# Kernel optimization log

Measured on AMD Instinct MI355X. Metric: run time of the kernel, lower is better.

Reference implementation:

```python
import jax, jax.numpy as jnp
import numpy as np

K_GAUSS = 10
HIDDEN = 512


def setup_inputs() -> dict:
    key = jax.random.key(0)
    k1, k2, k3 = jax.random.split(key, 3)
    lstm_out = jax.random.normal(k1, (16, 1024, HIDDEN), dtype=jnp.float32)
    char_seq = jax.random.uniform(k2, (16, 600, 80), dtype=jnp.float32)
    # Dense(3*k_gaussians): small init so exp(params) stays in a sane range
    W = jax.random.normal(k3, (HIDDEN, 3 * K_GAUSS), dtype=jnp.float32) * 0.02
    bias = jnp.zeros((3 * K_GAUSS,), dtype=jnp.float32)
    return {"lstm_out": lstm_out, "char_seq": char_seq, "W": W, "bias": bias}


def reference(lstm_out, char_seq, W, bias):
    # lstm_out: [B,T,H], char_seq: [B,U,A]
    U = char_seq.shape[1]
    params = jnp.einsum('bth,hp->btp', lstm_out, W) + bias  # [B,T,3K]
    exp_params = jnp.exp(params)
    a, b, k = jnp.split(exp_params, 3, axis=2)              # each [B,T,K]
    u = jnp.arange(U, dtype=lstm_out.dtype).reshape(1, 1, U, 1)  # char indices
    # gaussian mixture window weights phi[b,t,u] = sum_k a*exp(-b*(k-u)^2)
    gaussians = a[:, :, None, :] * jnp.exp(-b[:, :, None, :] * jnp.square(k[:, :, None, :] - u))  # [B,T,U,K]
    char_weights = jnp.sum(gaussians, axis=3)               # [B,T,U]
    # alphabet_window[b,t,a] = sum_u phi[b,t,u] * char_seq[b,u,a]
    return jnp.einsum('btu,bua->bta', char_weights, char_seq)
```

## Files before the change

kernel.cpp:

```cpp
#include <hip/hip_runtime.h>
#include <math.h>

#define BB 16
#define TD 1024
#define HD 512
#define UD 600
#define AD 80
#define KG 10
#define PC 30
#define PP 32

#define LOG2E 1.4426950408889634f

#if __has_builtin(__builtin_amdgcn_exp2f)
#define EXP2F(x) __builtin_amdgcn_exp2f(x)
#else
#define EXP2F(x) exp2f(x)
#endif

typedef short v8s __attribute__((ext_vector_type(8)));
typedef float v4f __attribute__((ext_vector_type(4)));

__device__ inline unsigned short f2bf(float f) {
    unsigned u = __float_as_uint(f);
    return (unsigned short)((u + 0x7FFF + ((u >> 16) & 1)) >> 16);
}

__global__ void k_wprep(const float* __restrict__ W,
                        unsigned short* __restrict__ Wfh,
                        unsigned short* __restrict__ Wfl) {
    int p = blockIdx.x * 256 + threadIdx.x;
    for (; p < 32768; p += 256 * 32) {
        int j = p & 7, l = (p >> 3) & 63, n = (p >> 9) & 1, kt = p >> 10;
        int k = kt * 32 + ((l >> 4) * 8) + j;
        int c = n * 16 + (l & 15);
        float v = (c < PC) ? W[k * PC + c] : 0.f;
        unsigned short h = f2bf(v);
        float hi_f = __uint_as_float(((unsigned)h) << 16);
        Wfh[p] = h;
        Wfl[p] = f2bf(v - hi_f);
    }
}

#define TT 16
#define UC 40
#define NCHUNK 15
#define NTHR 320

__global__ __launch_bounds__(NTHR, 4) void k_fused(const float* __restrict__ x,
                                                   const unsigned short* __restrict__ Wfh,
                                                   const unsigned short* __restrict__ Wfl,
                                                   const float* __restrict__ bias,
                                                   const float* __restrict__ cs,
                                                   float* __restrict__ out) {
    __shared__ float red[4 * TT * 33];
    __shared__ float params_l[TT * 36];
    __shared__ float cs_l[UC * AD];
    __shared__ float phi2[TT * 44];
    __shared__ float range_l[2];

    int tid = threadIdx.x;
    int b = blockIdx.y;
    int t0 = blockIdx.x * TT;
    long r0 = (long)b * TD + t0;

    int wv = tid >> 6;
    int l = tid & 63;
    int quad = l >> 4, m = l & 15;

    const float* csb = cs + (long)b * UD * AD;

    if (wv < 4) {
        v4f acc[2] = {{0.f, 0.f, 0.f, 0.f}, {0.f, 0.f, 0.f, 0.f}};

        #pragma unroll
        for (int kt = 0; kt < 4; kt++) {
            int g = wv * 4 + kt;
            const float* xr = x + (r0 + m) * HD + g * 32 + quad * 8;
            float4 xa = *(const float4*)(xr);
            float4 xb = *(const float4*)(xr + 4);
            float xf[8] = {xa.x, xa.y, xa.z, xa.w, xb.x, xb.y, xb.z, xb.w};
            v8s ah, al;
            #pragma unroll
            for (int j = 0; j < 8; j++) {
                unsigned short h = f2bf(xf[j]);
                ah[j] = (short)h;
                al[j] = (short)f2bf(xf[j] - __uint_as_float(((unsigned)h) << 16));
            }
            #pragma unroll
            for (int n = 0; n < 2; n++) {
                uint4 uh = *(const uint4*)&Wfh[((g * 2 + n) * 64 + l) * 8];
                uint4 ul = *(const uint4*)&Wfl[((g * 2 + n) * 64 + l) * 8];
                v8s bh, bl;
                __builtin_memcpy(&bh, &uh, 16);
                __builtin_memcpy(&bl, &ul, 16);
                acc[n] = __builtin_amdgcn_mfma_f32_16x16x32_bf16(ah, bh, acc[n], 0, 0, 0);
                acc[n] = __builtin_amdgcn_mfma_f32_16x16x32_bf16(al, bh, acc[n], 0, 0, 0);
                acc[n] = __builtin_amdgcn_mfma_f32_16x16x32_bf16(ah, bl, acc[n], 0, 0, 0);
            }
        }

        #pragma unroll
        for (int n = 0; n < 2; n++)
            #pragma unroll
            for (int r = 0; r < 4; r++)
                red[wv * (TT * 33) + (quad * 4 + r) * 33 + n * 16 + m] = acc[n][r];
    } else {
        for (int idx = l; idx < (UC * AD) / 4; idx += 64)
            *(float4*)&cs_l[idx * 4] = *(const float4*)&csb[idx * 4];
    }
    __syncthreads();

    for (int idx = tid; idx < TT * PC; idx += NTHR) {
        int r = idx / PC, c = idx - r * PC;
        float s = red[0 * (TT * 33) + r * 33 + c] + red[1 * (TT * 33) + r * 33 + c]
                + red[2 * (TT * 33) + r * 33 + c] + red[3 * (TT * 33) + r * 33 + c];
        float e = __expf(s + bias[c]);
        params_l[r * 36 + c] = (c >= 10 && c < 20) ? (-e * LOG2E) : e;
    }
    __syncthreads();

    int tt = tid & 15;
    int sub = tid >> 4;
    float pa[KG], pnb[KG], pk[KG];
    #pragma unroll
    for (int q = 0; q < KG; q++) {
        pa[q]  = params_l[tt * 36 + q];
        pnb[q] = params_l[tt * 36 + 10 + q];
        pk[q]  = params_l[tt * 36 + 20 + q];
    }

    {
        float lo = 1e30f, hi = -1e30f;
        #pragma unroll
        for (int q = 0; q < KG; q++) {
            float bits = 46.f + fmaxf(0.f, __log2f(pa[q]));
            float w = __fsqrt_rn(bits / (-pnb[q]));
            lo = fminf(lo, pk[q] - w);
            hi = fmaxf(hi, pk[q] + w);
        }
        if (tid < 64) {
            #pragma unroll
            for (int mk = 1; mk < 64; mk <<= 1) {
                lo = fminf(lo, __shfl_xor(lo, mk));
                hi = fmaxf(hi, __shfl_xor(hi, mk));
            }
            if (tid == 0) { range_l[0] = lo; range_l[1] = hi; }
        }
    }
    __syncthreads();
    float lo_m = fminf(fmaxf(range_l[0], 0.f), (float)(UD - 1));
    float hi_m = fminf(fmaxf(range_l[1], 0.f), (float)(UD - 1));
    int ch_lo = (int)lo_m / UC;
    int ch_hi = (int)hi_m / UC;
    if (ch_lo > ch_hi) ch_lo = ch_hi;

    int tx = tid % 20;
    int ty = tid / 20;
    float4 acc0 = {0.f, 0.f, 0.f, 0.f};

    for (int ch = ch_lo; ch <= ch_hi; ch++) {
        int u0 = ch * UC;
        __syncthreads();

        if (ch != 0) {
            for (int idx = tid; idx < (UC * AD) / 4; idx += NTHR) {
                *(float4*)&cs_l[idx * 4] = *(const float4*)&csb[u0 * AD + idx * 4];
            }
        }

        float ph[2];
        #pragma unroll
        for (int i = 0; i < 2; i++) {
            float uf = (float)(u0 + sub * 2 + i);
            float ss = 0.f;
            #pragma unroll
            for (int q = 0; q < KG; q++) {
                float d = uf - pk[q];
                ss += pa[q] * EXP2F(pnb[q] * d * d);
            }
            ph[i] = ss;
        }
        *(float2*)&phi2[tt * 44 + sub * 2] = make_float2(ph[0], ph[1]);
        __syncthreads();

        #pragma unroll 2
        for (int g = 0; g < 10; g++) {
            float4 p0 = *(const float4*)&phi2[ty * 44 + g * 4];
            #pragma unroll
            for (int i = 0; i < 4; i++) {
                float4 c4 = *(const float4*)&cs_l[(g * 4 + i) * AD + tx * 4];
                float pi0 = (i == 0) ? p0.x : (i == 1) ? p0.y : (i == 2) ? p0.z : p0.w;
                acc0.x += pi0 * c4.x; acc0.y += pi0 * c4.y;
                acc0.z += pi0 * c4.z; acc0.w += pi0 * c4.w;
            }
        }
    }

    *(float4*)(out + (r0 + ty) * AD + tx * 4) = acc0;
}

extern "C" void kernel_launch(void* const* d_in, const int* in_sizes, int n_in,
                              void* d_out, int out_size, void* d_ws, size_t ws_size,
                              hipStream_t stream) {
    const float* lstm = (const float*)d_in[0];
    const float* cs   = (const float*)d_in[1];
    const float* W    = (const float*)d_in[2];
    const float* bias = (const float*)d_in[3];
    float* out = (float*)d_out;

    unsigned short* Wfh = (unsigned short*)d_ws;
    unsigned short* Wfl = Wfh + 32768;

    k_wprep<<<32, 256, 0, stream>>>(W, Wfh, Wfl);
    dim3 grid(TD / TT, BB);
    k_fused<<<grid, NTHR, 0, stream>>>(lstm, Wfh, Wfl, bias, cs, out);
}
```

Before: 89.60 us.

## Fold W bf16 split into fused kernel and drop separate prep launch

Removes the k_wprep kernel that pre-split W into bf16 hi/lo fragments, and instead has each MFMA wave load fp32 W directly and split it in-register. The MFMA operand roles are swapped (W as A, x as B), so the accumulator is transposed and the reduction buffer layout changes to match. The bf16 conversion now uses packed hardware conversion. This saves a kernel launch and the workspace round trip, at the cost of strided scalar W loads and redundant conversion work in every block.

Result: no change. 90.54 us (+1.0%).

```diff
diff --git a/kernel.cpp b/kernel.cpp
--- a/kernel.cpp
+++ b/kernel.cpp
@@ -1,4 +1,5 @@
 #include <hip/hip_runtime.h>
+#include <hip/hip_bf16.h>
 #include <math.h>
 
 #define BB 16
@@ -8,7 +9,6 @@
 #define AD 80
 #define KG 10
 #define PC 30
-#define PP 32
 
 #define LOG2E 1.4426950408889634f
 
@@ -21,25 +21,26 @@
 typedef short v8s __attribute__((ext_vector_type(8)));
 typedef float v4f __attribute__((ext_vector_type(4)));
 
-__device__ inline unsigned short f2bf(float f) {
-    unsigned u = __float_as_uint(f);
-    return (unsigned short)((u + 0x7FFF + ((u >> 16) & 1)) >> 16);
-}
-
-__global__ void k_wprep(const float* __restrict__ W,
-                        unsigned short* __restrict__ Wfh,
-                        unsigned short* __restrict__ Wfl) {
-    int p = blockIdx.x * 256 + threadIdx.x;
-    for (; p < 32768; p += 256 * 32) {
-        int j = p & 7, l = (p >> 3) & 63, n = (p >> 9) & 1, kt = p >> 10;
-        int k = kt * 32 + ((l >> 4) * 8) + j;
-        int c = n * 16 + (l & 15);
-        float v = (c < PC) ? W[k * PC + c] : 0.f;
-        unsigned short h = f2bf(v);
-        float hi_f = __uint_as_float(((unsigned)h) << 16);
-        Wfh[p] = h;
-        Wfl[p] = f2bf(v - hi_f);
-    }
+__device__ inline unsigned pk2bf(float a, float b) {
+    __hip_bfloat162 h = __float22bfloat162_rn(make_float2(a, b));
+    unsigned u;
+    __builtin_memcpy(&u, &h, 4);
+    return u;
+}
+
+__device__ inline void split8(const float* f, v8s& hi, v8s& lo) {
+    unsigned uh[4], ul[4];
+    #pragma unroll
+    for (int p = 0; p < 4; p++) {
+        float a = f[2 * p], b = f[2 * p + 1];
+        unsigned u = pk2bf(a, b);
+        uh[p] = u;
+        float ha = __uint_as_float(u << 16);
+        float hb = __uint_as_float(u & 0xFFFF0000u);
+        ul[p] = pk2bf(a - ha, b - hb);
+    }
+    __builtin_memcpy(&hi, uh, 16);
+    __builtin_memcpy(&lo, ul, 16);
 }
 
 #define TT 16
@@ -48,12 +49,11 @@
 #define NTHR 320
 
 __global__ __launch_bounds__(NTHR, 4) void k_fused(const float* __restrict__ x,
-                                                   const unsigned short* __restrict__ Wfh,
-                                                   const unsigned short* __restrict__ Wfl,
+                                                   const float* __restrict__ W,
                                                    const float* __restrict__ bias,
                                                    const float* __restrict__ cs,
                                                    float* __restrict__ out) {
-    __shared__ float red[4 * TT * 33];
+    __shared__ float red[4 * 32 * 17];
     __shared__ float params_l[TT * 36];
     __shared__ float cs_l[UC * AD];
     __shared__ float phi2[TT * 44];
@@ -76,35 +76,36 @@
         #pragma unroll
         for (int kt = 0; kt < 4; kt++) {
             int g = wv * 4 + kt;
+
             const float* xr = x + (r0 + m) * HD + g * 32 + quad * 8;
-            float4 xa = *(const float4*)(xr);
-            float4 xb = *(const float4*)(xr + 4);
-            float xf[8] = {xa.x, xa.y, xa.z, xa.w, xb.x, xb.y, xb.z, xb.w};
-            v8s ah, al;
-            #pragma unroll
-            for (int j = 0; j < 8; j++) {
-                unsigned short h = f2bf(xf[j]);
-                ah[j] = (short)h;
-                al[j] = (short)f2bf(xf[j] - __uint_as_float(((unsigned)h) << 16));
-            }
-            #pragma unroll
-            for (int n = 0; n < 2; n++) {
-                uint4 uh = *(const uint4*)&Wfh[((g * 2 + n) * 64 + l) * 8];
-                uint4 ul = *(const uint4*)&Wfl[((g * 2 + n) * 64 + l) * 8];
-                v8s bh, bl;
-                __builtin_memcpy(&bh, &uh, 16);
-                __builtin_memcpy(&bl, &ul, 16);
-                acc[n] = __builtin_amdgcn_mfma_f32_16x16x32_bf16(ah, bh, acc[n], 0, 0, 0);
-                acc[n] = __builtin_amdgcn_mfma_f32_16x16x32_bf16(al, bh, acc[n], 0, 0, 0);
-                acc[n] = __builtin_amdgcn_mfma_f32_16x16x32_bf16(ah, bl, acc[n], 0, 0, 0);
-            }
-        }
-
-        #pragma unroll
-        for (int n = 0; n < 2; n++)
+            float xf[8];
+            *(float4*)&xf[0] = *(const float4*)(xr);
+            *(float4*)&xf[4] = *(const float4*)(xr + 4);
+            v8s bh, bl;
+            split8(xf, bh, bl);
+
+            #pragma unroll
+            for (int ct = 0; ct < 2; ct++) {
+                int c = ct * 16 + m;
+                float wf[8] = {0.f, 0.f, 0.f, 0.f, 0.f, 0.f, 0.f, 0.f};
+                if (c < PC) {
+                    const float* wr = W + (long)(g * 32 + quad * 8) * PC + c;
+                    #pragma unroll
+                    for (int j = 0; j < 8; j++) wf[j] = wr[j * PC];
+                }
+                v8s ah, al;
+                split8(wf, ah, al);
+                acc[ct] = __builtin_amdgcn_mfma_f32_16x16x32_bf16(ah, bh, acc[ct], 0, 0, 0);
+                acc[ct] = __builtin_amdgcn_mfma_f32_16x16x32_bf16(al, bh, acc[ct], 0, 0, 0);
+                acc[ct] = __builtin_amdgcn_mfma_f32_16x16x32_bf16(ah, bl, acc[ct], 0, 0, 0);
+            }
+        }
+
+        #pragma unroll
+        for (int ct = 0; ct < 2; ct++)
             #pragma unroll
             for (int r = 0; r < 4; r++)
-                red[wv * (TT * 33) + (quad * 4 + r) * 33 + n * 16 + m] = acc[n][r];
+                red[wv * (32 * 17) + (ct * 16 + quad * 4 + r) * 17 + m] = acc[ct][r];
     } else {
         for (int idx = l; idx < (UC * AD) / 4; idx += 64)
             *(float4*)&cs_l[idx * 4] = *(const float4*)&csb[idx * 4];
@@ -112,11 +113,11 @@
     __syncthreads();
 
     for (int idx = tid; idx < TT * PC; idx += NTHR) {
-        int r = idx / PC, c = idx - r * PC;
-        float s = red[0 * (TT * 33) + r * 33 + c] + red[1 * (TT * 33) + r * 33 + c]
-                + red[2 * (TT * 33) + r * 33 + c] + red[3 * (TT * 33) + r * 33 + c];
+        int t = idx & 15, c = idx >> 4;
+        float s = red[0 * (32 * 17) + c * 17 + t] + red[1 * (32 * 17) + c * 17 + t]
+                + red[2 * (32 * 17) + c * 17 + t] + red[3 * (32 * 17) + c * 17 + t];
         float e = __expf(s + bias[c]);
-        params_l[r * 36 + c] = (c >= 10 && c < 20) ? (-e * LOG2E) : e;
+        params_l[t * 36 + c] = (c >= 10 && c < 20) ? (-e * LOG2E) : e;
     }
     __syncthreads();
 
@@ -209,10 +210,6 @@
     const float* bias = (const float*)d_in[3];
     float* out = (float*)d_out;
 
-    unsigned short* Wfh = (unsigned short*)d_ws;
-    unsigned short* Wfl = Wfh + 32768;
-
-    k_wprep<<<32, 256, 0, stream>>>(W, Wfh, Wfl);
     dim3 grid(TD / TT, BB);
-    k_fused<<<grid, NTHR, 0, stream>>>(lstm, Wfh, Wfl, bias, cs, out);
-}
+    k_fused<<<grid, NTHR, 0, stream>>>(lstm, W, bias, cs, out);
+}
```
